# Kernel optimization log

Measured on AMD Instinct MI355X. Metric: run time of the kernel, lower is better.

Reference implementation:

```python
import jax, jax.numpy as jnp
import numpy as np

N_NODES = 100000
N_EDGES = 3200000
F_IN = 128
HID = 256
EMB = 128
N_GRAPHS = 2048
N_CLASSES = 2


def _glorot(key, fan_in, fan_out):
    scale = np.sqrt(2.0 / (fan_in + fan_out)).astype(np.float32)
    return jax.random.normal(key, (fan_in, fan_out), jnp.float32) * scale


def setup_inputs() -> dict:
    key = jax.random.key(0)
    ks = jax.random.split(key, 12)
    x = jax.random.normal(ks[0], (N_NODES, F_IN), jnp.float32)
    edge_index = jax.random.randint(ks[1], (2, N_EDGES), 0, N_NODES, dtype=jnp.int64)
    batch = jnp.sort(jax.random.randint(ks[2], (N_NODES,), 0, N_GRAPHS, dtype=jnp.int64))
    return {
        "x": x,
        "edge_index": edge_index,
        "batch": batch,
        # GCN layer weights (input->hid, hid->hid, hid->emb)
        "W1": _glorot(ks[3], F_IN, HID), "b1": jnp.zeros((HID,), jnp.float32),
        "W2": _glorot(ks[4], HID, HID), "b2": jnp.zeros((HID,), jnp.float32),
        "W3": _glorot(ks[5], HID, EMB), "b3": jnp.zeros((EMB,), jnp.float32),
        # MLP classifier head
        "Wc1": _glorot(ks[6], EMB, HID), "bc1": jnp.zeros((HID,), jnp.float32),
        "Wc2": _glorot(ks[7], HID, HID // 2), "bc2": jnp.zeros((HID // 2,), jnp.float32),
        "Wc3": _glorot(ks[8], HID // 2, N_CLASSES), "bc3": jnp.zeros((N_CLASSES,), jnp.float32),
    }


def _gcn_conv(x, W, b, src, dst, dinv):
    # GCNConv with self loops: out = D^{-1/2}(A+I)D^{-1/2} (x @ W) + b
    h = x @ W  # [N, out]
    norm_e = dinv[src] * dinv[dst]  # [E]
    msg = h[src] * norm_e[:, None]
    agg = jax.ops.segment_sum(msg, dst, num_segments=N_NODES)
    agg = agg + h * (dinv * dinv)[:, None]  # self-loop term
    return agg + b


def reference(x, edge_index, batch, W1, b1, W2, b2, W3, b3, Wc1, bc1, Wc2, bc2, Wc3, bc3):
    src, dst = edge_index[0], edge_index[1]
    # degree including self loop (shared across layers)
    deg = jax.ops.segment_sum(jnp.ones((N_EDGES,), x.dtype), dst, num_segments=N_NODES) + 1.0
    dinv = jax.lax.rsqrt(deg)

    h = jax.nn.relu(_gcn_conv(x, W1, b1, src, dst, dinv))
    h = jax.nn.relu(_gcn_conv(h, W2, b2, src, dst, dinv))
    h = _gcn_conv(h, W3, b3, src, dst, dinv)  # final layer: no activation

    # mean pooling per graph
    sums = jax.ops.segment_sum(h, batch, num_segments=N_GRAPHS)  # [G, EMB]
    counts = jax.ops.segment_sum(jnp.ones((N_NODES,), h.dtype), batch, num_segments=N_GRAPHS)
    pooled = sums / jnp.maximum(counts, 1.0)[:, None]

    # MLP head (dropout is identity at eval)
    z = jax.nn.relu(pooled @ Wc1 + bc1)
    z = jax.nn.relu(z @ Wc2 + bc2)
    logits = z @ Wc3 + bc3  # [G, num_classes]
    return logits
```

## Files before the change

kernel.cpp:

```cpp
#include <hip/hip_runtime.h>
#include <cstdint>
#include <cstddef>

#define NODES  100000
#define EDGES  3200000
#define FIN    128
#define HIDDEN 256
#define EMBD   128
#define GRAPHS 2048

#define NB   256
#define NPB  391
#define CAP  16384
#define TILE 4096

typedef _Float16 f16;
typedef f16 f16x2 __attribute__((ext_vector_type(2)));
typedef f16 f16x4 __attribute__((ext_vector_type(4)));
typedef f16 f16x8 __attribute__((ext_vector_type(8)));
typedef float f32x4 __attribute__((ext_vector_type(4)));
typedef unsigned int u32;

__global__ __launch_bounds__(256) void binA_k(const int* __restrict__ src,
                                              const int* __restrict__ dst,
                                              u32* __restrict__ staging,
                                              int* __restrict__ gcur) {
  __shared__ u32 buf[TILE];
  __shared__ int bcnt[NB], bsh[NB], bstart[NB], bcur[NB], gbase[NB];
  const int tid = threadIdx.x;
  const int tb = blockIdx.x * TILE;

  bcnt[tid] = 0;
  __syncthreads();

#pragma unroll
  for (int j = 0; j < TILE / 256; ++j) {
    int i = tb + j * 256 + tid;
    if (i < EDGES) atomicAdd(&bcnt[dst[i] / NPB], 1);
  }
  __syncthreads();

  bsh[tid] = bcnt[tid];
  __syncthreads();
  for (int off = 1; off < NB; off <<= 1) {
    int t = (tid >= off) ? bsh[tid - off] : 0;
    __syncthreads();
    bsh[tid] += t;
    __syncthreads();
  }
  bstart[tid] = bsh[tid] - bcnt[tid];
  bcur[tid] = bsh[tid] - bcnt[tid];
  __syncthreads();

#pragma unroll
  for (int j = 0; j < TILE / 256; ++j) {
    int i = tb + j * 256 + tid;
    if (i < EDGES) {
      int d = dst[i];
      int b = d / NPB;
      u32 w = ((u32)src[i] << 9) | (u32)(d - b * NPB);
      buf[atomicAdd(&bcur[b], 1)] = w;
    }
  }
  gbase[tid] = atomicAdd(&gcur[tid], bcnt[tid]);
  __syncthreads();

  {
    int c = bcnt[tid], st = bstart[tid];
    u32* outp = staging + (size_t)tid * CAP + gbase[tid];
    for (int k = 0; k < c; ++k) outp[k] = buf[st + k];
  }
}

__global__ void bscan_k(const int* __restrict__ gcur, int* __restrict__ bbase) {
  __shared__ int sh[NB];
  int tid = threadIdx.x;
  int v = gcur[tid];
  sh[tid] = v;
  __syncthreads();
  for (int off = 1; off < NB; off <<= 1) {
    int t = (tid >= off) ? sh[tid - off] : 0;
    __syncthreads();
    sh[tid] += t;
    __syncthreads();
  }
  bbase[tid] = sh[tid] - v;
}

__global__ __launch_bounds__(512) void binB_k(const u32* __restrict__ staging,
                                              const int* __restrict__ gcur,
                                              const int* __restrict__ bbase,
                                              int* __restrict__ row_ptr,
                                              float* __restrict__ dinv,
                                              int* __restrict__ csr_src) {
  __shared__ int ncnt[512];
  __shared__ int ncur[512];
  const int b = blockIdx.x;
  const int tid = threadIdx.x;
  const int m = gcur[b];
  const int base = bbase[b];
  const int nb0 = b * NPB;
  const int nn = min(NPB, NODES - nb0);
  const u32* sb = staging + (size_t)b * CAP;

  ncnt[tid] = 0;
  __syncthreads();

  for (int k = tid; k < m; k += 512) atomicAdd(&ncnt[sb[k] & 511], 1);
  __syncthreads();

  int v = ncnt[tid];
  for (int off = 1; off < 512; off <<= 1) {
    int t = (tid >= off) ? ncnt[tid - off] : 0;
    __syncthreads();
    ncnt[tid] += t;
    __syncthreads();
  }
  int incl = ncnt[tid];
  if (tid < nn) {
    row_ptr[nb0 + tid + 1] = base + incl;
    dinv[nb0 + tid] = rsqrtf((float)(v + 1));
    ncur[tid] = base + incl - v;
  }
  if (b == 0 && tid == 0) row_ptr[0] = 0;
  __syncthreads();

  for (int k = tid; k < m; k += 512) {
    u32 w = sb[k];
    int pos = atomicAdd(&ncur[w & 511], 1);
    csr_src[pos] = (int)(w >> 9);
  }
}

__global__ void prescale_k(const float* __restrict__ x, const float* __restrict__ dinv,
                           f16* __restrict__ xs) {
  int idx = blockIdx.x * blockDim.x + threadIdx.x;
  if (idx >= NODES * FIN / 4) return;
  int row = idx >> 5;
  float4 v = *(const float4*)(x + (size_t)idx * 4);
  float d = dinv[row];
  f16x4 o = {(f16)(d * v.x), (f16)(d * v.y), (f16)(d * v.z), (f16)(d * v.w)};
  *(f16x4*)(xs + (size_t)idx * 4) = o;
}

__global__ void convw3_k(const float* __restrict__ W1, const float* __restrict__ W2,
                         const float* __restrict__ W3, f16* __restrict__ Wt1,
                         f16* __restrict__ Wt2, f16* __restrict__ Wt3) {
  int i = blockIdx.x * blockDim.x + threadIdx.x;
  if (i < 32768) {
    int k = i >> 8, m = i & 255;
    Wt1[(size_t)m * FIN + k] = (f16)W1[i];
  } else if (i < 98304) {
    int j = i - 32768;
    int k = j >> 8, m = j & 255;
    Wt2[(size_t)m * HIDDEN + k] = (f16)W2[j];
  } else if (i < 131072) {
    int j = i - 98304;
    int k = j >> 7, m = j & 127;
    Wt3[(size_t)m * HIDDEN + k] = (f16)W3[j];
  }
}

template <int V, bool FINAL>
__global__ __launch_bounds__(256) void agg_h(const f16* __restrict__ in, void* __restrict__ outv,
                      const int* __restrict__ row_ptr, const int* __restrict__ csr_src,
                      const float* __restrict__ dinv, const float* __restrict__ bias) {
  constexpr int D = V * 32;
  constexpr int U = 8;
  const int wid = (blockIdx.x * blockDim.x + threadIdx.x) >> 6;
  const int half = (threadIdx.x >> 5) & 1;
  const int lane = threadIdx.x & 31;
  const int node = wid * 2 + half;
  if (node >= NODES) return;
  const int c0 = lane * V;
  const f16* __restrict__ inc = in + c0;

  float acc[V];
#pragma unroll
  for (int v = 0; v < V; ++v) acc[v] = 0.f;

  const int beg = row_ptr[node], end = row_ptr[node + 1];
  int k = beg;
  if constexpr (V == 8) {
    for (; k + U <= end; k += U) {
      int s[U];
#pragma unroll
      for (int u = 0; u < U; ++u) s[u] = csr_src[k + u];
      f16x8 hv[U];
#pragma unroll
      for (int u = 0; u < U; ++u) hv[u] = *(const f16x8*)(inc + (size_t)s[u] * D);
#pragma unroll
      for (int u = 0; u < U; ++u)
#pragma unroll
        for (int v = 0; v < V; ++v) acc[v] += (float)hv[u][v];
    }
    for (; k < end; ++k) {
      f16x8 hv = *(const f16x8*)(inc + (size_t)csr_src[k] * D);
#pragma unroll
      for (int v = 0; v < V; ++v) acc[v] += (float)hv[v];
    }
    f16x8 hv = *(const f16x8*)(inc + (size_t)node * D);
#pragma unroll
    for (int v = 0; v < V; ++v) acc[v] += (float)hv[v];
  } else {
    for (; k + U <= end; k += U) {
      int s[U];
#pragma unroll
      for (int u = 0; u < U; ++u) s[u] = csr_src[k + u];
      f16x4 hv[U];
#pragma unroll
      for (int u = 0; u < U; ++u) hv[u] = *(const f16x4*)(inc + (size_t)s[u] * D);
#pragma unroll
      for (int u = 0; u < U; ++u)
#pragma unroll
        for (int v = 0; v < V; ++v) acc[v] += (float)hv[u][v];
    }
    for (; k < end; ++k) {
      f16x4 hv = *(const f16x4*)(inc + (size_t)csr_src[k] * D);
#pragma unroll
      for (int v = 0; v < V; ++v) acc[v] += (float)hv[v];
    }
    f16x4 hv = *(const f16x4*)(inc + (size_t)node * D);
#pragma unroll
    for (int v = 0; v < V; ++v) acc[v] += (float)hv[v];
  }

  const float di = dinv[node];
  if constexpr (FINAL) {
    float* out = (float*)outv;
    float4 o = {di * acc[0] + bias[c0], di * acc[1] + bias[c0 + 1],
                di * acc[2] + bias[c0 + 2], di * acc[3] + bias[c0 + 3]};
    *(float4*)(out + (size_t)node * D + c0) = o;
  } else {
    f16* out = (f16*)outv;
    if constexpr (V == 8) {
      f16x8 o;
#pragma unroll
      for (int v = 0; v < V; ++v) o[v] = (f16)(di * acc[v]);
      *(f16x8*)(out + (size_t)node * D + c0) = o;
    } else {
      f16x4 o;
#pragma unroll
      for (int v = 0; v < V; ++v) o[v] = (f16)(di * acc[v]);
      *(f16x4*)(out + (size_t)node * D + c0) = o;
    }
  }
}

template <int K>
__global__ __launch_bounds__(256, 2) void gemm_w(const f16* __restrict__ A,
                                                 const f16* __restrict__ Wt,
                                                 const float* __restrict__ bias,
                                                 const float* __restrict__ dinv,
                                                 f16* __restrict__ C, int N) {
  constexpr int M = 256;
  __shared__ f16 As[128][40];
  __shared__ f16 Bs[256][40];

  const int tid = threadIdx.x;
  const int rowbase = blockIdx.x * 128;
  const int l = tid & 63;
  const int wv = tid >> 6;
  const int wr = (wv >> 1) * 64;
  const int wc = (wv & 1) * 128;
  const int lr = tid >> 1;
  const int lc = (tid & 1) * 16;

  f32x4 acc[4][8];
#pragma unroll
  for (int i = 0; i < 4; ++i)
#pragma unroll
    for (int j = 0; j < 8; ++j) acc[i][j] = (f32x4){0.f, 0.f, 0.f, 0.f};

  const int arow = min(rowbase + lr, N - 1);
  const f16* aptr = A + (size_t)arow * K + lc;
  const f16* bptr = Wt + (size_t)tid * K;

  for (int kb = 0; kb < K; kb += 32) {
    *(f16x8*)&As[lr][lc]     = *(const f16x8*)(aptr + kb);
    *(f16x8*)&As[lr][lc + 8] = *(const f16x8*)(aptr + kb + 8);
#pragma unroll
    for (int q = 0; q < 4; ++q)
      *(f16x8*)&Bs[tid][q * 8] = *(const f16x8*)(bptr + kb + q * 8);
    __syncthreads();

    f16x8 a[4], b[8];
#pragma unroll
    for (int f = 0; f < 4; ++f)
      a[f] = *(const f16x8*)&As[wr + f * 16 + (l & 15)][(l >> 4) * 8];
#pragma unroll
    for (int g = 0; g < 8; ++g)
      b[g] = *(const f16x8*)&Bs[wc + g * 16 + (l & 15)][(l >> 4) * 8];
#pragma unroll
    for (int fm = 0; fm < 4; ++fm)
#pragma unroll
      for (int g = 0; g < 8; ++g)
        acc[fm][g] = __builtin_amdgcn_mfma_f32_16x16x32_f16(a[fm], b[g], acc[fm][g], 0, 0, 0);
    __syncthreads();
  }

  float bv[8];
#pragma unroll
  for (int g = 0; g < 8; ++g) bv[g] = bias[wc + g * 16 + (l & 15)];

#pragma unroll
  for (int fm = 0; fm < 4; ++fm) {
#pragma unroll
    for (int r = 0; r < 4; ++r) {
      int row = rowbase + wr + fm * 16 + (l >> 4) * 4 + r;
      if (row >= N) continue;
      float dv = dinv[row];
#pragma unroll
      for (int g = 0; g < 8; ++g) {
        int col = wc + g * 16 + (l & 15);
        float v = fmaxf(acc[fm][g][r] + bv[g], 0.f);
        C[(size_t)row * M + col] = (f16)(v * dv);
      }
    }
  }
}

template <int K, bool RELU, bool BIAS, bool DSCALE>
__global__ __launch_bounds__(256) void gemm_h(const f16* __restrict__ A,
                                              const f16* __restrict__ Wt,
                                              const float* __restrict__ bias,
                                              const float* __restrict__ dinv,
                                              f16* __restrict__ C, int N, int M) {
  __shared__ f16 As[128][40];
  __shared__ f16 Bs[128][40];

  const int tid = threadIdx.x;
  const int rowbase = blockIdx.x * 128;
  const int colbase = blockIdx.y * 128;
  const int l = tid & 63;
  const int wr = ((tid >> 6) >> 1) * 64;
  const int wc = ((tid >> 6) & 1) * 64;
  const int lr = tid >> 1;
  const int lc = (tid & 1) * 16;

  f32x4 acc[4][4];
#pragma unroll
  for (int i = 0; i < 4; ++i)
#pragma unroll
    for (int j = 0; j < 4; ++j) acc[i][j] = (f32x4){0.f, 0.f, 0.f, 0.f};

  const int arow = min(rowbase + lr, N - 1);
  const f16* aptr = A + (size_t)arow * K + lc;
  const f16* bptr = Wt + (size_t)(colbase + lr) * K + lc;

  for (int kb = 0; kb < K; kb += 32) {
    *(f16x8*)&As[lr][lc]     = *(const f16x8*)(aptr + kb);
    *(f16x8*)&As[lr][lc + 8] = *(const f16x8*)(aptr + kb + 8);
    *(f16x8*)&Bs[lr][lc]     = *(const f16x8*)(bptr + kb);
    *(f16x8*)&Bs[lr][lc + 8] = *(const f16x8*)(bptr + kb + 8);
    __syncthreads();

    f16x8 a[4], b[4];
#pragma unroll
    for (int f = 0; f < 4; ++f) {
      a[f] = *(const f16x8*)&As[wr + f * 16 + (l & 15)][(l >> 4) * 8];
      b[f] = *(const f16x8*)&Bs[wc + f * 16 + (l & 15)][(l >> 4) * 8];
    }
#pragma unroll
    for (int fm = 0; fm < 4; ++fm)
#pragma unroll
      for (int fn = 0; fn < 4; ++fn)
        acc[fm][fn] = __builtin_amdgcn_mfma_f32_16x16x32_f16(a[fm], b[fn], acc[fm][fn], 0, 0, 0);
    __syncthreads();
  }

  float bv[4];
#pragma unroll
  for (int fn = 0; fn < 4; ++fn)
    bv[fn] = BIAS ? bias[colbase + wc + fn * 16 + (l & 15)] : 0.f;

#pragma unroll
  for (int fm = 0; fm < 4; ++fm) {
#pragma unroll
    for (int r = 0; r < 4; ++r) {
      int row = rowbase + wr + fm * 16 + (l >> 4) * 4 + r;
      if (row >= N) continue;
      float dv = DSCALE ? dinv[row] : 1.f;
#pragma unroll
      for (int fn = 0; fn < 4; ++fn) {
        int col = colbase + wc + fn * 16 + (l & 15);
        float v = acc[fm][fn][r] + bv[fn];
        if (RELU) v = fmaxf(v, 0.f);
        C[(size_t)row * M + col] = (f16)(v * dv);
      }
    }
  }
}

template <int K, bool RELU, bool HAS_BIAS>
__global__ __launch_bounds__(256) void gemm_k(const float* __restrict__ A,
                                              const float* __restrict__ W,
                                              const float* __restrict__ bias,
                                              float* __restrict__ C, int N, int M) {
  constexpr int KB = 16;
  __shared__ float As[KB][128];
  __shared__ float Ws[KB][128];

  const int tid = threadIdx.x;
  const int rowbase = blockIdx.x * 128;
  const int colbase = blockIdx.y * 128;
  const int tr = tid >> 4;
  const int tc = tid & 15;
  const int ar = tid >> 1;
  const int ac4_0 = (tid & 1) * 2;
  const int wk = tid >> 4;
  const int wc4_0 = (tid & 15) * 2;

  float acc[8][8];
#pragma unroll
  for (int i = 0; i < 8; ++i)
#pragma unroll
    for (int j = 0; j < 8; ++j) acc[i][j] = 0.f;

  for (int kb = 0; kb < K; kb += KB) {
#pragma unroll
    for (int q = 0; q < 2; ++q) {
      int c4 = ac4_0 + q;
      int grow = rowbase + ar;
      float4 v = make_float4(0.f, 0.f, 0.f, 0.f);
      if (grow < N) v = *(const float4*)(A + (size_t)grow * K + kb + c4 * 4);
      As[c4 * 4 + 0][ar] = v.x;
      As[c4 * 4 + 1][ar] = v.y;
      As[c4 * 4 + 2][ar] = v.z;
      As[c4 * 4 + 3][ar] = v.w;
    }
#pragma unroll
    for (int q = 0; q < 2; ++q) {
      int c4 = wc4_0 + q;
      float4 v = *(const float4*)(W + (size_t)(kb + wk) * M + colbase + c4 * 4);
      *(float4*)&Ws[wk][c4 * 4] = v;
    }
    __syncthreads();

#pragma unroll
    for (int kk = 0; kk < KB; ++kk) {
      float4 a0 = *(const float4*)&As[kk][tr * 4];
      float4 a1 = *(const float4*)&As[kk][tr * 4 + 64];
      float4 w0 = *(const float4*)&Ws[kk][tc * 4];
      float4 w1 = *(const float4*)&Ws[kk][tc * 4 + 64];
      float a[8] = {a0.x, a0.y, a0.z, a0.w, a1.x, a1.y, a1.z, a1.w};
      float w[8] = {w0.x, w0.y, w0.z, w0.w, w1.x, w1.y, w1.z, w1.w};
#pragma unroll
      for (int i = 0; i < 8; ++i)
#pragma unroll
        for (int j = 0; j < 8; ++j) acc[i][j] = fmaf(a[i], w[j], acc[i][j]);
    }
    __syncthreads();
  }

#pragma unroll
  for (int i = 0; i < 8; ++i) {
    int r = rowbase + ((i < 4) ? (tr * 4 + i) : (64 + tr * 4 + (i - 4)));
    if (r >= N) continue;
#pragma unroll
    for (int jh = 0; jh < 2; ++jh) {
      int c = colbase + tc * 4 + jh * 64;
      float4 o;
      o.x = acc[i][jh * 4 + 0];
      o.y = acc[i][jh * 4 + 1];
      o.z = acc[i][jh * 4 + 2];
      o.w = acc[i][jh * 4 + 3];
      if (HAS_BIAS) {
        o.x += bias[c]; o.y += bias[c + 1]; o.z += bias[c + 2]; o.w += bias[c + 3];
      }
      if (RELU) {
        o.x = fmaxf(o.x, 0.f); o.y = fmaxf(o.y, 0.f);
        o.z = fmaxf(o.z, 0.f); o.w = fmaxf(o.w, 0.f);
      }
      *(float4*)(C + (size_t)r * M + c) = o;
    }
  }
}

__global__ void pool_k(const float* __restrict__ h, const int* __restrict__ batch,
                       float* __restrict__ pooled) {
  int g = blockIdx.x;
  int j = threadIdx.x;
  int lo = 0, hi = NODES;
  while (lo < hi) { int mid = (lo + hi) >> 1; if (batch[mid] < g) lo = mid + 1; else hi = mid; }
  int start = lo;
  int lo2 = start, hi2 = NODES;
  while (lo2 < hi2) { int mid = (lo2 + hi2) >> 1; if (batch[mid] < g + 1) lo2 = mid + 1; else hi2 = mid; }
  int end = lo2;
  float s = 0.f;
  for (int r = start; r < end; ++r) s += h[(size_t)r * EMBD + j];
  float c = (float)(end - start);
  pooled[g * EMBD + j] = s / fmaxf(c, 1.f);
}

__global__ void head_k(const float* __restrict__ z2, const float* __restrict__ Wc3,
                       const float* __restrict__ bc3, float* __restrict__ out) {
  int wv = (blockIdx.x * blockDim.x + threadIdx.x) >> 6;
  int lane = threadIdx.x & 63;
  if (wv >= GRAPHS) return;
  float2 z = *(const float2*)(z2 + (size_t)wv * 128 + lane * 2);
  int j0 = lane * 2;
  float a0 = z.x * Wc3[j0 * 2 + 0] + z.y * Wc3[(j0 + 1) * 2 + 0];
  float a1 = z.x * Wc3[j0 * 2 + 1] + z.y * Wc3[(j0 + 1) * 2 + 1];
  for (int off = 32; off; off >>= 1) {
    a0 += __shfl_down(a0, off);
    a1 += __shfl_down(a1, off);
  }
  if (lane == 0) {
    out[wv * 2 + 0] = a0 + bc3[0];
    out[wv * 2 + 1] = a1 + bc3[1];
  }
}

extern "C" void kernel_launch(void* const* d_in, const int* in_sizes, int n_in,
                              void* d_out, int out_size, void* d_ws, size_t ws_size,
                              hipStream_t stream) {
  const float* x    = (const float*)d_in[0];
  const int*   ei   = (const int*)d_in[1];
  const int*   batch= (const int*)d_in[2];
  const float* W1 = (const float*)d_in[3];  const float* b1 = (const float*)d_in[4];
  const float* W2 = (const float*)d_in[5];  const float* b2 = (const float*)d_in[6];
  const float* W3 = (const float*)d_in[7];  const float* b3 = (const float*)d_in[8];
  const float* Wc1= (const float*)d_in[9];  const float* bc1= (const float*)d_in[10];
  const float* Wc2= (const float*)d_in[11]; const float* bc2= (const float*)d_in[12];
  const float* Wc3= (const float*)d_in[13]; const float* bc3= (const float*)d_in[14];
  float* out = (float*)d_out;

  char* ws = (char*)d_ws;
  size_t off = 0;
  auto alloc = [&](size_t bytes) -> void* {
    void* p = ws + off;
    off = (off + bytes + 255) & ~(size_t)255;
    return p;
  };
  f16*   F0      = (f16*)alloc((size_t)NODES * 256 * 2);
  f16*   F1      = (f16*)alloc((size_t)NODES * 256 * 2);
  float* R0      = (float*)alloc((size_t)NODES * 128 * 4);
  int*   csr_src = (int*)alloc((size_t)EDGES * 4);
  u32*   staging = (u32*)alloc((size_t)NB * CAP * 4);
  int*   row_ptr = (int*)alloc((size_t)(NODES + 1) * 4);
  float* dinv    = (float*)alloc((size_t)NODES * 4);
  int*   gcur    = (int*)alloc(NB * 4);
  int*   bbase   = (int*)alloc(NB * 4);
  f16*   Wt1     = (f16*)alloc((size_t)FIN * HIDDEN * 2);
  f16*   Wt2     = (f16*)alloc((size_t)HIDDEN * HIDDEN * 2);
  f16*   Wt3     = (f16*)alloc((size_t)HIDDEN * EMBD * 2);
  float* pooled = (float*)F0;
  float* z1     = pooled + (size_t)GRAPHS * EMBD;
  float* z2     = z1 + (size_t)GRAPHS * HIDDEN;

  const int* srcA = ei;
  const int* dstA = ei + EDGES;

  hipMemsetAsync(gcur, 0, NB * 4, stream);
  binA_k<<<(EDGES + TILE - 1) / TILE, 256, 0, stream>>>(srcA, dstA, staging, gcur);
  bscan_k<<<1, NB, 0, stream>>>(gcur, bbase);
  binB_k<<<NB, 512, 0, stream>>>(staging, gcur, bbase, row_ptr, dinv, csr_src);

  convw3_k<<<(131072 + 255) / 256, 256, 0, stream>>>(W1, W2, W3, Wt1, Wt2, Wt3);
  prescale_k<<<(NODES * FIN / 4 + 255) / 256, 256, 0, stream>>>(x, dinv, F0);

  const int aggBlocks = ((NODES + 1) / 2 * 64 + 255) / 256;
  const int gemmRows = (NODES + 127) / 128;

  agg_h<4, false><<<aggBlocks, 256, 0, stream>>>(F0, F1, row_ptr, csr_src, dinv, nullptr);
  gemm_w<FIN><<<gemmRows, 256, 0, stream>>>(F1, Wt1, b1, dinv, F0, NODES);
  agg_h<8, false><<<aggBlocks, 256, 0, stream>>>(F0, F1, row_ptr, csr_src, dinv, nullptr);
  gemm_w<HIDDEN><<<gemmRows, 256, 0, stream>>>(F1, Wt2, b2, dinv, F0, NODES);
  gemm_h<HIDDEN, false, false, false><<<dim3(gemmRows, 1), 256, 0, stream>>>(F0, Wt3, nullptr, nullptr, F1, NODES, EMBD);
  agg_h<4, true><<<aggBlocks, 256, 0, stream>>>(F1, R0, row_ptr, csr_src, dinv, b3);

  pool_k<<<GRAPHS, 128, 0, stream>>>(R0, batch, pooled);
  gemm_k<EMBD, true, true><<<dim3((GRAPHS + 127) / 128, 2), 256, 0, stream>>>(pooled, Wc1, bc1, z1, GRAPHS, HIDDEN);
  gemm_k<HIDDEN, true, true><<<dim3((GRAPHS + 127) / 128, 1), 256, 0, stream>>>(z1, Wc2, bc2, z2, GRAPHS, EMBD);
  head_k<<<GRAPHS / 4, 256, 0, stream>>>(z2, Wc3, bc3, out);
}
```

Measured before the change: 705.5 us.

## Fuse input prescale into CSR build, store final layer in fp16, enlarge bin tile

```diff
diff --git a/kernel.cpp b/kernel.cpp
--- a/kernel.cpp
+++ b/kernel.cpp
@@ -12,7 +12,7 @@
 #define NB   256
 #define NPB  391
 #define CAP  16384
-#define TILE 4096
+#define TILE 8192
 
 typedef _Float16 f16;
 typedef f16 f16x2 __attribute__((ext_vector_type(2)));
@@ -92,9 +92,12 @@
                                               const int* __restrict__ bbase,
                                               int* __restrict__ row_ptr,
                                               float* __restrict__ dinv,
-                                              int* __restrict__ csr_src) {
+                                              int* __restrict__ csr_src,
+                                              const float* __restrict__ x,
+                                              f16* __restrict__ xs) {
   __shared__ int ncnt[512];
   __shared__ int ncur[512];
+  __shared__ float sdinv[512];
   const int b = blockIdx.x;
   const int tid = threadIdx.x;
   const int m = gcur[b];
@@ -117,9 +120,11 @@
     __syncthreads();
   }
   int incl = ncnt[tid];
+  float dv = rsqrtf((float)(v + 1));
   if (tid < nn) {
     row_ptr[nb0 + tid + 1] = base + incl;
-    dinv[nb0 + tid] = rsqrtf((float)(v + 1));
+    dinv[nb0 + tid] = dv;
+    sdinv[tid] = dv;
     ncur[tid] = base + incl - v;
   }
   if (b == 0 && tid == 0) row_ptr[0] = 0;
@@ -130,17 +135,15 @@
     int pos = atomicAdd(&ncur[w & 511], 1);
     csr_src[pos] = (int)(w >> 9);
   }
-}
-
-__global__ void prescale_k(const float* __restrict__ x, const float* __restrict__ dinv,
-                           f16* __restrict__ xs) {
-  int idx = blockIdx.x * blockDim.x + threadIdx.x;
-  if (idx >= NODES * FIN / 4) return;
-  int row = idx >> 5;
-  float4 v = *(const float4*)(x + (size_t)idx * 4);
-  float d = dinv[row];
-  f16x4 o = {(f16)(d * v.x), (f16)(d * v.y), (f16)(d * v.z), (f16)(d * v.w)};
-  *(f16x4*)(xs + (size_t)idx * 4) = o;
+
+  for (int idx = tid; idx < nn * 32; idx += 512) {
+    int row = idx >> 5;
+    int c4 = idx & 31;
+    float d = sdinv[row];
+    float4 vx = *(const float4*)(x + (size_t)(nb0 + row) * FIN + c4 * 4);
+    f16x4 o = {(f16)(d * vx.x), (f16)(d * vx.y), (f16)(d * vx.z), (f16)(d * vx.w)};
+    *(f16x4*)(xs + (size_t)(nb0 + row) * FIN + c4 * 4) = o;
+  }
 }
 
 __global__ void convw3_k(const float* __restrict__ W1, const float* __restrict__ W2,
@@ -162,7 +165,7 @@
 }
 
 template <int V, bool FINAL>
-__global__ __launch_bounds__(256) void agg_h(const f16* __restrict__ in, void* __restrict__ outv,
+__global__ __launch_bounds__(256) void agg_h(const f16* __restrict__ in, f16* __restrict__ out,
                       const int* __restrict__ row_ptr, const int* __restrict__ csr_src,
                       const float* __restrict__ dinv, const float* __restrict__ bias) {
   constexpr int D = V * 32;
@@ -227,12 +230,11 @@
 
   const float di = dinv[node];
   if constexpr (FINAL) {
-    float* out = (float*)outv;
-    float4 o = {di * acc[0] + bias[c0], di * acc[1] + bias[c0 + 1],
-                di * acc[2] + bias[c0 + 2], di * acc[3] + bias[c0 + 3]};
-    *(float4*)(out + (size_t)node * D + c0) = o;
+    f16x4 o;
+#pragma unroll
+    for (int v = 0; v < V; ++v) o[v] = (f16)(di * acc[v] + bias[c0 + v]);
+    *(f16x4*)(out + (size_t)node * D + c0) = o;
   } else {
-    f16* out = (f16*)outv;
     if constexpr (V == 8) {
       f16x8 o;
 #pragma unroll
@@ -477,7 +479,7 @@
   }
 }
 
-__global__ void pool_k(const float* __restrict__ h, const int* __restrict__ batch,
+__global__ void pool_k(const f16* __restrict__ h, const int* __restrict__ batch,
                        float* __restrict__ pooled) {
   int g = blockIdx.x;
   int j = threadIdx.x;
@@ -488,7 +490,7 @@
   while (lo2 < hi2) { int mid = (lo2 + hi2) >> 1; if (batch[mid] < g + 1) lo2 = mid + 1; else hi2 = mid; }
   int end = lo2;
   float s = 0.f;
-  for (int r = start; r < end; ++r) s += h[(size_t)r * EMBD + j];
+  for (int r = start; r < end; ++r) s += (float)h[(size_t)r * EMBD + j];
   float c = (float)(end - start);
   pooled[g * EMBD + j] = s / fmaxf(c, 1.f);
 }
@@ -535,7 +537,7 @@
   };
   f16*   F0      = (f16*)alloc((size_t)NODES * 256 * 2);
   f16*   F1      = (f16*)alloc((size_t)NODES * 256 * 2);
-  float* R0      = (float*)alloc((size_t)NODES * 128 * 4);
+  f16*   hbuf    = (f16*)alloc((size_t)NODES * 128 * 2);
   int*   csr_src = (int*)alloc((size_t)EDGES * 4);
   u32*   staging = (u32*)alloc((size_t)NB * CAP * 4);
   int*   row_ptr = (int*)alloc((size_t)(NODES + 1) * 4);
@@ -545,7 +547,7 @@
   f16*   Wt1     = (f16*)alloc((size_t)FIN * HIDDEN * 2);
   f16*   Wt2     = (f16*)alloc((size_t)HIDDEN * HIDDEN * 2);
   f16*   Wt3     = (f16*)alloc((size_t)HIDDEN * EMBD * 2);
-  float* pooled = (float*)F0;
+  float* pooled = (float*)F1;
   float* z1     = pooled + (size_t)GRAPHS * EMBD;
   float* z2     = z1 + (size_t)GRAPHS * HIDDEN;
 
@@ -555,10 +557,9 @@
   hipMemsetAsync(gcur, 0, NB * 4, stream);
   binA_k<<<(EDGES + TILE - 1) / TILE, 256, 0, stream>>>(srcA, dstA, staging, gcur);
   bscan_k<<<1, NB, 0, stream>>>(gcur, bbase);
-  binB_k<<<NB, 512, 0, stream>>>(staging, gcur, bbase, row_ptr, dinv, csr_src);
+  binB_k<<<NB, 512, 0, stream>>>(staging, gcur, bbase, row_ptr, dinv, csr_src, x, F0);
 
   convw3_k<<<(131072 + 255) / 256, 256, 0, stream>>>(W1, W2, W3, Wt1, Wt2, Wt3);
-  prescale_k<<<(NODES * FIN / 4 + 255) / 256, 256, 0, stream>>>(x, dinv, F0);
 
   const int aggBlocks = ((NODES + 1) / 2 * 64 + 255) / 256;
   const int gemmRows = (NODES + 127) / 128;
@@ -568,9 +569,9 @@
   agg_h<8, false><<<aggBlocks, 256, 0, stream>>>(F0, F1, row_ptr, csr_src, dinv, nullptr);
   gemm_w<HIDDEN><<<gemmRows, 256, 0, stream>>>(F1, Wt2, b2, dinv, F0, NODES);
   gemm_h<HIDDEN, false, false, false><<<dim3(gemmRows, 1), 256, 0, stream>>>(F0, Wt3, nullptr, nullptr, F1, NODES, EMBD);
-  agg_h<4, true><<<aggBlocks, 256, 0, stream>>>(F1, R0, row_ptr, csr_src, dinv, b3);
-
-  pool_k<<<GRAPHS, 128, 0, stream>>>(R0, batch, pooled);
+  agg_h<4, true><<<aggBlocks, 256, 0, stream>>>(F1, hbuf, row_ptr, csr_src, dinv, b3);
+
+  pool_k<<<GRAPHS, 128, 0, stream>>>(hbuf, batch, pooled);
   gemm_k<EMBD, true, true><<<dim3((GRAPHS + 127) / 128, 2), 256, 0, stream>>>(pooled, Wc1, bc1, z1, GRAPHS, HIDDEN);
   gemm_k<HIDDEN, true, true><<<dim3((GRAPHS + 127) / 128, 1), 256, 0, stream>>>(z1, Wc2, bc2, z2, GRAPHS, EMBD);
   head_k<<<GRAPHS / 4, 256, 0, stream>>>(z2, Wc3, bc3, out);
```

Result: no change. 694.5 us (-1.6%).
